# Kernel tuning notes

Measured on AMD Instinct MI355X. Metric: run time of the kernel, lower is better.

Reference implementation:

```python
import jax, jax.numpy as jnp
import numpy as np

GAMMA = 2.0
CONTEXT_WINDOW = 100


def setup_inputs() -> dict:
    key = jax.random.key(0)
    k1, k2 = jax.random.split(key)
    B, S, C = 64, 131072, 3
    inputs = jax.random.normal(k1, (B, S, C), dtype=jnp.float32)
    targets = jax.random.randint(k2, (B, S), 0, C, dtype=jnp.int32)
    alpha = jnp.array([0.25, 1.0, 1.0], dtype=jnp.float32)
    return {"inputs": inputs, "targets": targets, "alpha": alpha}


def _window_mask(targets, window):
    # mask[b, i] = True iff any positive target within +/- window of i;
    # rows with no positives are fully True (matches torch loop semantics).
    B, S = targets.shape
    pos = targets > 0                                   # (B, S) bool
    cs = jnp.cumsum(pos.astype(jnp.int32), axis=1)      # inclusive prefix sums
    c = jnp.concatenate([jnp.zeros((B, 1), jnp.int32), cs], axis=1)  # (B, S+1)
    idx = jnp.arange(S)
    hi = jnp.minimum(idx + window + 1, S)               # exclusive end
    lo = jnp.maximum(idx - window, 0)                   # inclusive start
    count = c[:, hi] - c[:, lo]                         # positives in window
    mask = count > 0
    has_pos = pos.any(axis=1, keepdims=True)
    return jnp.where(has_pos, mask, True)


def reference(inputs, targets, alpha):
    # inputs: (B, S, C) logits; targets: (B, S) class indices
    mask = _window_mask(targets, CONTEXT_WINDOW)                     # (B, S)
    logp = jax.nn.log_softmax(inputs, axis=-1)                       # (B, S, C)
    ce = -jnp.take_along_axis(logp, targets[..., None].astype(jnp.int32), axis=-1)[..., 0]
    p_t = jnp.exp(-ce)
    focal = alpha[targets] * (1.0 - p_t) ** GAMMA * ce               # (B, S)
    m = mask.astype(inputs.dtype)
    # masked mean == mean over selected elements in the torch version
    return jnp.sum(focal * m) / jnp.sum(m)
```

## Files before the change

### kernel.cpp

```cpp
#include <hip/hip_runtime.h>

#define BB 64
#define SS 131072
#define WIN 100
#define TILE 4096
#define NTHREADS 256
#define NWAVES (NTHREADS / 64)
#define TILES_PER_ROW (SS / TILE)
#define NBLOCKS (BB * TILES_PER_ROW)
#define EXT (TILE + 2*WIN)
#define NWORDS ((EXT + 63) / 64)
#define SH_BYTES (NWORDS * 64)
#define K4TOT (SH_BYTES / 4)
#define SROUNDS ((K4TOT + NTHREADS - 1) / NTHREADS)
#define WGROUPS 4
#define GF4 192

typedef float  fx4 __attribute__((ext_vector_type(4)));
typedef int    ix4 __attribute__((ext_vector_type(4)));

__global__ __launch_bounds__(NTHREADS, 6) void focal_main(
    const float* __restrict__ inputs, const int* __restrict__ targets,
    const float* __restrict__ alpha, double* __restrict__ slots)
{
    __shared__ __align__(16) unsigned char sh_t[SH_BYTES];
    __shared__ unsigned long long wbits[NWORDS];
    __shared__ unsigned long long mbits[NWORDS];
    __shared__ fx4 lbuf[NWAVES][GF4];
    __shared__ double red[NWAVES * 4];

    const int t = threadIdx.x;
    const int w = t >> 6, l = t & 63;
    const int b = blockIdx.x / TILES_PER_ROW;
    const int tile = blockIdx.x % TILES_PER_ROW;
    const int s0 = tile * TILE;
    const int ext_lo = (s0 - WIN > 0) ? (s0 - WIN) : 0;
    const int ext_hi = (s0 + TILE + WIN < SS) ? (s0 + TILE + WIN) : SS;
    const int ext_len = ext_hi - ext_lo;
    const int tr_lo = s0 - ext_lo;

    const float* inrow = inputs + (long)b * SS * 3;
    const fx4* gsrc = (const fx4*)(inrow + (long)(s0 + w * 1024) * 3);
    fx4 q0 = __builtin_nontemporal_load(gsrc + l);
    fx4 q1 = __builtin_nontemporal_load(gsrc + 64 + l);
    fx4 q2 = __builtin_nontemporal_load(gsrc + 128 + l);

    const int* trow = targets + (long)b * SS;
    #pragma unroll
    for (int it = 0; it < SROUNDS; ++it) {
        const int k4 = it * NTHREADS + t;
        if (k4 < K4TOT) {
            unsigned int pk = 0;
            if (4 * k4 < ext_len) {
                const ix4 tv4 =
                    __builtin_nontemporal_load((const ix4*)(trow + ext_lo + 4 * k4));
                pk = (unsigned)(tv4.x & 3) | ((unsigned)(tv4.y & 3) << 8) |
                     ((unsigned)(tv4.z & 3) << 16) | ((unsigned)(tv4.w & 3) << 24);
            }
            ((unsigned int*)sh_t)[k4] = pk;
        }
    }
    __syncthreads();

    int cnt_p = 0;
    if (t < NWORDS) {
        const uint4* qp = (const uint4*)(sh_t + (t << 6));
        unsigned long long wv = 0;
        #pragma unroll
        for (int r = 0; r < 4; ++r) {
            const uint4 u = qp[r];
            unsigned int x, nz;
            x = u.x; nz = (x | (x >> 1)) & 0x01010101u;
            wv |= (unsigned long long)((nz * 0x01020408u) >> 24) << (r*16 + 0);
            x = u.y; nz = (x | (x >> 1)) & 0x01010101u;
            wv |= (unsigned long long)((nz * 0x01020408u) >> 24) << (r*16 + 4);
            x = u.z; nz = (x | (x >> 1)) & 0x01010101u;
            wv |= (unsigned long long)((nz * 0x01020408u) >> 24) << (r*16 + 8);
            x = u.w; nz = (x | (x >> 1)) & 0x01010101u;
            wv |= (unsigned long long)((nz * 0x01020408u) >> 24) << (r*16 + 12);
        }
        wbits[t] = wv;
        int lo_bit = tr_lo - (t << 6);        if (lo_bit < 0) lo_bit = 0;
        int hi_bit = tr_lo + TILE - (t << 6); if (hi_bit > 64) hi_bit = 64;
        if (hi_bit > lo_bit) {
            unsigned long long rm = (hi_bit >= 64) ? ~0ULL : ((1ULL << hi_bit) - 1);
            rm &= (~0ULL << lo_bit);
            cnt_p = __popcll(wv & rm);
        }
    }
    __syncthreads();

    if (t < NWORDS) {
        const unsigned long long a = (t >= 2) ? wbits[t-2] : 0ULL;
        const unsigned long long bw = (t >= 1) ? wbits[t-1] : 0ULL;
        const unsigned long long c = wbits[t];
        const unsigned long long d = (t+1 < NWORDS) ? wbits[t+1] : 0ULL;
        const unsigned long long e = (t+2 < NWORDS) ? wbits[t+2] : 0ULL;
        unsigned long long m = c ? ~0ULL : 0ULL;
        if (d) { const int lo = __builtin_ctzll(d) - 36;
                 m |= (lo <= 0) ? ~0ULL : (~0ULL << lo); }
        if (e) { const int lo = __builtin_ctzll(e) + 28;
                 if (lo <= 63) m |= (~0ULL << lo); }
        if (bw) { const int hi = 63 - __builtin_clzll(bw) + 36;
                  m |= (hi >= 63) ? ~0ULL : (~0ULL >> (63 - hi)); }
        if (a) { const int hi = 63 - __builtin_clzll(a) - 28;
                 if (hi >= 0) m |= (hi >= 63) ? ~0ULL : (~0ULL >> (63 - hi)); }
        mbits[t] = m;
    }
    __syncthreads();

    const float a0 = alpha[0], a1 = alpha[1], a2 = alpha[2];
    float fsum_m = 0.0f, fsum_a = 0.0f;
    int cnt_m = 0;

    #pragma unroll
    for (int g = 0; g < WGROUPS; ++g) {
        fx4* pb = lbuf[w];
        pb[l] = q0; pb[64 + l] = q1; pb[128 + l] = q2;
        if (g + 1 < WGROUPS) {
            const fx4* gn = gsrc + (g + 1) * GF4;
            q0 = __builtin_nontemporal_load(gn + l);
            q1 = __builtin_nontemporal_load(gn + 64 + l);
            q2 = __builtin_nontemporal_load(gn + 128 + l);
        }
        const fx4 c0 = pb[3 * l];
        const fx4 c1 = pb[3 * l + 1];
        const fx4 c2 = pb[3 * l + 2];

        const int j0 = tr_lo + w * 1024 + g * 256 + l * 4;
        const unsigned long long mw = mbits[j0 >> 6];
        const unsigned int tpack = *(const unsigned int*)(sh_t + j0);
        const float xs[12] = {c0.x, c0.y, c0.z, c0.w, c1.x, c1.y, c1.z, c1.w,
                              c2.x, c2.y, c2.z, c2.w};
        #pragma unroll
        for (int j = 0; j < 4; ++j) {
            const float x0 = xs[3*j], x1 = xs[3*j+1], x2 = xs[3*j+2];
            const int tv = (tpack >> (8 * j)) & 0xFF;
            const float mx = fmaxf(x0, fmaxf(x1, x2));
            const float mn = fminf(x0, fminf(x1, x2));
            const float md = fmaxf(fminf(x0, x1), fminf(fmaxf(x0, x1), x2));
            const float emd = __expf(md - mx);
            const float emn = __expf(mn - mx);
            const float sum = 1.0f + emd + emn;
            const float xt  = (tv == 0) ? x0 : ((tv == 1) ? x1 : x2);
            const float ce  = __logf(sum) + (mx - xt);
            const float pt  = __expf(-ce);
            const float wgt = (tv == 0) ? a0 : ((tv == 1) ? a1 : a2);
            const float om  = 1.0f - pt;
            const float focal = wgt * om * om * ce;
            const bool  msk = (mw >> ((j0 & 63) + j)) & 1ULL;
            fsum_a += focal;
            fsum_m += msk ? focal : 0.0f;
            cnt_m  += msk ? 1 : 0;
        }
    }

    #pragma unroll
    for (int off = 32; off >= 1; off >>= 1) {
        fsum_m += __shfl_down(fsum_m, off);
        fsum_a += __shfl_down(fsum_a, off);
        cnt_m  += __shfl_down(cnt_m, off);
        cnt_p  += __shfl_down(cnt_p, off);
    }
    if (l == 0) {
        red[w*4]   = (double)fsum_m; red[w*4+1] = (double)cnt_m;
        red[w*4+2] = (double)fsum_a; red[w*4+3] = (double)cnt_p;
    }
    __syncthreads();
    if (t == 0) {
        double sm = 0, sc = 0, sa = 0, sp = 0;
        #pragma unroll
        for (int v = 0; v < NWAVES; ++v) {
            sm += red[v*4]; sc += red[v*4+1]; sa += red[v*4+2]; sp += red[v*4+3];
        }
        double* slot = slots + (long)blockIdx.x * 4;
        slot[0] = sm;
        slot[1] = sc;
        slot[2] = sa;
        slot[3] = sp;
    }
}

__global__ __launch_bounds__(1024) void focal_final(
    const double* __restrict__ slots, float* __restrict__ out)
{
    __shared__ double redA[16 * 2];
    __shared__ double crs[BB];
    __shared__ double crc[BB];
    const int t = threadIdx.x;
    const int wave = t >> 6, lane = t & 63;

    double sm = 0.0, sc = 0.0;
    for (int k = t; k < NBLOCKS; k += 1024) {
        sm += slots[(long)k * 4 + 0];
        sc += slots[(long)k * 4 + 1];
    }
    #pragma unroll
    for (int off = 32; off >= 1; off >>= 1) {
        sm += __shfl_down(sm, off);
        sc += __shfl_down(sc, off);
    }
    if (lane == 0) { redA[wave*2] = sm; redA[wave*2+1] = sc; }

    const int row = t >> 4;
    const int rpart = t & 15;
    const long base = (long)row * TILES_PER_ROW + rpart * 2;
    double rs = slots[base*4 + 2] + slots[(base+1)*4 + 2];
    double rp = slots[base*4 + 3] + slots[(base+1)*4 + 3];
    #pragma unroll
    for (int off = 8; off >= 1; off >>= 1) {
        rs += __shfl_down(rs, off, 16);
        rp += __shfl_down(rp, off, 16);
    }
    if (rpart == 0) { crs[row] = rs; crc[row] = rp; }
    __syncthreads();

    if (t == 0) {
        double a = 0.0, bsum = 0.0;
        #pragma unroll
        for (int v = 0; v < 16; ++v) { a += redA[v*2]; bsum += redA[v*2+1]; }
        double corr_s = 0.0, corr_c = 0.0;
        #pragma unroll
        for (int r = 0; r < BB; ++r) {
            if (crc[r] == 0.0) { corr_s += crs[r]; corr_c += (double)SS; }
        }
        out[0] = (float)((a + corr_s) / (bsum + corr_c));
    }
}

extern "C" void kernel_launch(void* const* d_in, const int* in_sizes, int n_in,
                              void* d_out, int out_size, void* d_ws, size_t ws_size,
                              hipStream_t stream) {
    const float* inputs  = (const float*)d_in[0];
    const int*   targets = (const int*)d_in[1];
    const float* alpha   = (const float*)d_in[2];
    float* out = (float*)d_out;

    double* slots = (double*)d_ws;

    focal_main<<<NBLOCKS, NTHREADS, 0, stream>>>(inputs, targets, alpha, slots);
    focal_final<<<1, 1024, 0, stream>>>(slots, out);
}
```

Measured before the change: 166.1 us.

## Stream logits directly into LDS with global_load_lds DMA instead of register staging

```diff
diff --git a/kernel.cpp b/kernel.cpp
--- a/kernel.cpp
+++ b/kernel.cpp
@@ -14,19 +14,31 @@
 #define K4TOT (SH_BYTES / 4)
 #define SROUNDS ((K4TOT + NTHREADS - 1) / NTHREADS)
 #define WGROUPS 4
-#define GF4 192
+#define GFLOATS 768
 
 typedef float  fx4 __attribute__((ext_vector_type(4)));
 typedef int    ix4 __attribute__((ext_vector_type(4)));
 
-__global__ __launch_bounds__(NTHREADS, 6) void focal_main(
+__device__ __forceinline__ void dma_group(const float* gp, float* lp, int l) {
+    __builtin_amdgcn_global_load_lds(
+        (const __attribute__((address_space(1))) float*)(gp + (l << 2)),
+        (__attribute__((address_space(3))) float*)(lp), 16, 0, 0);
+    __builtin_amdgcn_global_load_lds(
+        (const __attribute__((address_space(1))) float*)(gp + 256 + (l << 2)),
+        (__attribute__((address_space(3))) float*)(lp + 256), 16, 0, 0);
+    __builtin_amdgcn_global_load_lds(
+        (const __attribute__((address_space(1))) float*)(gp + 512 + (l << 2)),
+        (__attribute__((address_space(3))) float*)(lp + 512), 16, 0, 0);
+}
+
+__global__ __launch_bounds__(NTHREADS, 8) void focal_main(
     const float* __restrict__ inputs, const int* __restrict__ targets,
     const float* __restrict__ alpha, double* __restrict__ slots)
 {
     __shared__ __align__(16) unsigned char sh_t[SH_BYTES];
     __shared__ unsigned long long wbits[NWORDS];
     __shared__ unsigned long long mbits[NWORDS];
-    __shared__ fx4 lbuf[NWAVES][GF4];
+    __shared__ __align__(16) float lbuf[NWAVES][GFLOATS];
     __shared__ double red[NWAVES * 4];
 
     const int t = threadIdx.x;
@@ -40,10 +52,9 @@
     const int tr_lo = s0 - ext_lo;
 
     const float* inrow = inputs + (long)b * SS * 3;
-    const fx4* gsrc = (const fx4*)(inrow + (long)(s0 + w * 1024) * 3);
-    fx4 q0 = __builtin_nontemporal_load(gsrc + l);
-    fx4 q1 = __builtin_nontemporal_load(gsrc + 64 + l);
-    fx4 q2 = __builtin_nontemporal_load(gsrc + 128 + l);
+    const float* gsrc = inrow + (long)(s0 + w * 1024) * 3;
+    float* lbase = &lbuf[w][0];
+    dma_group(gsrc, lbase, l);
 
     const int* trow = targets + (long)b * SS;
     #pragma unroll
@@ -112,20 +123,17 @@
     const float a0 = alpha[0], a1 = alpha[1], a2 = alpha[2];
     float fsum_m = 0.0f, fsum_a = 0.0f;
     int cnt_m = 0;
+    const fx4* lread = (const fx4*)lbase;
 
     #pragma unroll
     for (int g = 0; g < WGROUPS; ++g) {
-        fx4* pb = lbuf[w];
-        pb[l] = q0; pb[64 + l] = q1; pb[128 + l] = q2;
-        if (g + 1 < WGROUPS) {
-            const fx4* gn = gsrc + (g + 1) * GF4;
-            q0 = __builtin_nontemporal_load(gn + l);
-            q1 = __builtin_nontemporal_load(gn + 64 + l);
-            q2 = __builtin_nontemporal_load(gn + 128 + l);
-        }
-        const fx4 c0 = pb[3 * l];
-        const fx4 c1 = pb[3 * l + 1];
-        const fx4 c2 = pb[3 * l + 2];
+        asm volatile("s_waitcnt vmcnt(0)" ::: "memory");
+        const fx4 c0 = lread[3 * l];
+        const fx4 c1 = lread[3 * l + 1];
+        const fx4 c2 = lread[3 * l + 2];
+        asm volatile("s_waitcnt lgkmcnt(0)" ::: "memory");
+        if (g + 1 < WGROUPS)
+            dma_group(gsrc + (g + 1) * GFLOATS, lbase, l);
 
         const int j0 = tr_lo + w * 1024 + g * 256 + l * 4;
         const unsigned long long mw = mbits[j0 >> 6];
```

Result: slower. 178.3 us (+7.4%).
